# Performance work log

Measured on AMD Instinct MI355X. Metric: run time of the kernel, lower is better.

## Reference

```python
import jax, jax.numpy as jnp
import numpy as np

KSIZE = 3
SCALE = 10.0
EPS = 1e-4


def _prelu(x, a):
    return jnp.where(x >= 0, x, a * x)


def _conv1x1(x, w, b):
    # x: [B,C,H,W], w: [O,C], b: [O]
    return jnp.einsum('bchw,oc->bohw', x, w) + b[None, :, None, None]


def _extract_patches(x, k):
    # same-padded kxk patches, torch-unfold channel-major ordering.
    # x: [B,C,H,W] -> [B, H*W, C, k, k]
    B, C, H, W = x.shape
    p = k // 2
    xp = jnp.pad(x, ((0, 0), (0, 0), (p, p), (p, p)))
    pats = jnp.stack([xp[:, :, i:i + H, j:j + W]
                      for i in range(k) for j in range(k)], axis=2)  # [B,C,k*k,H,W]
    pats = pats.reshape(B, C, k, k, H * W)
    return jnp.transpose(pats, (0, 4, 1, 2, 3))


def setup_inputs() -> dict:
    key = jax.random.key(0)
    ks = jax.random.split(key, 10)
    B, C, r = 4, 64, 2
    H = W = 96
    h = w = 48
    Cr = C // r
    s = 0.05
    return {
        'input': jax.random.normal(ks[0], (B, C, H, W), jnp.float32),
        'small': jax.random.normal(ks[1], (B, C, h, w), jnp.float32),
        'w_match1': jax.random.normal(ks[2], (Cr, C), jnp.float32) * s,
        'b_match1': jax.random.normal(ks[3], (Cr,), jnp.float32) * s,
        'a_match1': jnp.full((1,), 0.25, jnp.float32),
        'w_match2': jax.random.normal(ks[4], (Cr, C), jnp.float32) * s,
        'b_match2': jax.random.normal(ks[5], (Cr,), jnp.float32) * s,
        'a_match2': jnp.full((1,), 0.25, jnp.float32),
        'w_asm': jax.random.normal(ks[6], (C, C), jnp.float32) * s,
        'b_asm': jax.random.normal(ks[7], (C,), jnp.float32) * s,
        'a_asm': jnp.full((1,), 0.25, jnp.float32),
    }


def reference(input, small, w_match1, b_match1, a_match1,
              w_match2, b_match2, a_match2, w_asm, b_asm, a_asm):
    dn = ('NCHW', 'OIHW', 'NCHW')
    pad1 = [(1, 1), (1, 1)]

    match_input = _prelu(_conv1x1(input, w_match1, b_match1), a_match1)  # [B,Cr,H,W]
    embed_w = _prelu(_conv1x1(small, w_asm, b_asm), a_asm)               # [B,C,h,w]
    ref = _prelu(_conv1x1(small, w_match2, b_match2), a_match2)          # [B,Cr,h,w]

    raw_w = _extract_patches(embed_w, KSIZE)  # [B, L, C, 3, 3]  (reconstruction filters)
    w_pat = _extract_patches(ref, KSIZE)      # [B, L, Cr, 3, 3] (matching filters)

    def per_sample(xi, wi, raw_wi):
        # xi: [Cr,H,W], wi: [L,Cr,3,3], raw_wi: [L,C,3,3]
        norm = jnp.sqrt(jnp.sum(wi * wi, axis=(1, 2, 3), keepdims=True))
        wi_n = wi / jnp.maximum(norm, EPS)
        # dynamic conv: correlation of xi with all L normalized patches
        yi = jax.lax.conv_general_dilated(xi[None], wi_n, (1, 1), pad1,
                                          dimension_numbers=dn)  # [1,L,H,W]
        yi = jax.nn.softmax(yi * SCALE, axis=1)
        # conv_transpose2d(yi, raw_wi, stride=2, padding=1):
        # lhs_dilation=2, pad k-1-p=1, spatially flipped, in/out swapped kernel
        wt = jnp.transpose(raw_wi, (1, 0, 2, 3))[:, :, ::-1, ::-1]  # [C,L,3,3]
        out = jax.lax.conv_general_dilated(yi, wt, (1, 1), pad1,
                                           lhs_dilation=(2, 2),
                                           dimension_numbers=dn)  # [1,C,2H-1,2W-1]
        return out[0] / 6.0

    return jax.vmap(per_sample)(match_input, w_pat, raw_w)
```

## Files before the change

kernel.cpp:

```cpp
#include <hip/hip_runtime.h>


typedef unsigned short u16;
typedef __attribute__((ext_vector_type(8))) short short8;
typedef __attribute__((ext_vector_type(8))) _Float16 half8;
typedef __attribute__((ext_vector_type(4))) float f32x4;

__device__ __forceinline__ u16 f2bf(float f) {
    unsigned u = __float_as_uint(f);
    unsigned r = (u + 0x7FFFu + ((u >> 16) & 1u)) >> 16;
    return (u16)r;
}
__device__ __forceinline__ float bf2f(u16 h) {
    return __uint_as_float(((unsigned)h) << 16);
}
__device__ __forceinline__ u16 f2h(float f) {
    _Float16 h = (_Float16)f;
    u16 u; __builtin_memcpy(&u, &h, 2); return u;
}
__device__ __forceinline__ float h2f(u16 u) {
    _Float16 h; __builtin_memcpy(&h, &u, 2); return (float)h;
}

__global__ void kzero(float4* p, long n) {
    long i = (long)blockIdx.x * blockDim.x + threadIdx.x;
    long st = (long)gridDim.x * blockDim.x;
    float4 z; z.x = 0.f; z.y = 0.f; z.z = 0.f; z.w = 0.f;
    for (; i < n; i += st) p[i] = z;
}

__global__ void kmatch(const float* __restrict__ input, const float* __restrict__ w1,
                       const float* __restrict__ b1, const float* __restrict__ a1,
                       u16* __restrict__ xf16) {
    __shared__ float xl[64 * 96];
    __shared__ float wl[32 * 65];
    int b = blockIdx.x / 96, y = blockIdx.x % 96;
    int tid = threadIdx.x;
    for (int i = tid; i < 64 * 96; i += 256) {
        int ci = i / 96, xx = i % 96;
        xl[i] = input[(((b * 64 + ci) * 96) + y) * 96 + xx];
    }
    for (int i = tid; i < 2048; i += 256) wl[(i >> 6) * 65 + (i & 63)] = w1[i];
    __syncthreads();
    float aa = a1[0];
    for (int o = tid; o < 96 * 32; o += 256) {
        int xx = o >> 5, c = o & 31;
        float acc = b1[c];
        #pragma unroll
        for (int ci = 0; ci < 64; ci++) acc = fmaf(xl[ci * 96 + xx], wl[c * 65 + ci], acc);
        float v = acc >= 0.f ? acc : aa * acc;
        xf16[((b * 98 + y + 1) * 98 + (xx + 1)) * 32 + c] = f2h(v);
    }
}

__global__ void ksmall(const float* __restrict__ small, const float* __restrict__ wasm,
                       const float* __restrict__ basm, const float* __restrict__ aasm,
                       const float* __restrict__ wm2, const float* __restrict__ bm2,
                       const float* __restrict__ am2,
                       float* __restrict__ ef32, u16* __restrict__ rkl) {
    __shared__ float sl[64 * 48];
    __shared__ float wa[64 * 65];
    __shared__ float wm[32 * 65];
    int b = blockIdx.x / 48, y = blockIdx.x % 48;
    int tid = threadIdx.x;
    for (int i = tid; i < 64 * 48; i += 256) {
        int ci = i / 48, xx = i % 48;
        sl[i] = small[(((b * 64 + ci) * 48) + y) * 48 + xx];
    }
    for (int i = tid; i < 4096; i += 256) wa[(i >> 6) * 65 + (i & 63)] = wasm[i];
    for (int i = tid; i < 2048; i += 256) wm[(i >> 6) * 65 + (i & 63)] = wm2[i];
    __syncthreads();
    float ae = aasm[0], ar = am2[0];
    for (int o = tid; o < 48 * 64; o += 256) {
        int xx = o >> 6, c = o & 63;
        float acc = basm[c];
        #pragma unroll
        for (int ci = 0; ci < 64; ci++) acc = fmaf(sl[ci * 48 + xx], wa[c * 65 + ci], acc);
        float v = acc >= 0.f ? acc : ae * acc;
        ef32[((b * 50 + y + 1) * 50 + (xx + 1)) * 64 + c] = v;
    }
    for (int o = tid; o < 48 * 32; o += 256) {
        int xx = o >> 5, c = o & 31;
        float acc = bm2[c];
        #pragma unroll
        for (int ci = 0; ci < 64; ci++) acc = fmaf(sl[ci * 48 + xx], wm[c * 65 + ci], acc);
        float v = acc >= 0.f ? acc : ar * acc;
        rkl[((b * 50 + y + 1) * 50 + (xx + 1)) * 32 + c] = f2h(v);
    }
}

__global__ void kinvnorm(const u16* __restrict__ rkl, float* __restrict__ invn) {
    int idx = blockIdx.x * 256 + threadIdx.x;
    int b = idx / 2304, l = idx % 2304;
    int ly = l / 48, lx = l % 48;
    float s = 0.f;
    for (int ty = 0; ty < 3; ty++)
        for (int tx = 0; tx < 3; tx++) {
            int base = ((b * 50 + ly + ty) * 50 + (lx + tx)) * 32;
            #pragma unroll
            for (int c = 0; c < 32; c++) {
                float v = h2f(rkl[base + c]);
                s = fmaf(v, v, s);
            }
        }
    invn[idx] = 10.f / fmaxf(sqrtf(s), 1e-4f);
}

__global__ void kvtp(const float* __restrict__ ef32, u16* __restrict__ vtp) {
    int bi = blockIdx.x;
    int b = bi / 576, n = bi % 576;
    int t = n >> 6, c = n & 63;
    int ty = t / 3, tx = t % 3;
    const float* eb = ef32 + (size_t)b * 50 * 50 * 64 + c;
    u16* vo = vtp + (size_t)(b * 576 + n) * 2304;
    for (int l = threadIdx.x; l < 2304; l += 256) {
        int ly = l / 48, lx = l - ly * 48;
        vo[l] = f2bf(eb[((ly + ty) * 50 + (lx + tx)) * 64]);
    }
}

__device__ __forceinline__ void stage_ks(const u16* __restrict__ src, u16* dst, int tid) {
    int wb = tid & ~63;
    #pragma unroll
    for (int k = 0; k < 3; ++k)
        __builtin_amdgcn_global_load_lds(
            (const __attribute__((address_space(1))) void*)(src + (size_t)(tid + k * 256) * 8),
            (__attribute__((address_space(3))) void*)(dst + (size_t)(wb + k * 256) * 8),
            16, 0, 0);
    if (tid < 32)
        __builtin_amdgcn_global_load_lds(
            (const __attribute__((address_space(1))) void*)(src + (size_t)(tid + 768) * 8),
            (__attribute__((address_space(3))) void*)(dst + (size_t)768 * 8),
            16, 0, 0);
}

__launch_bounds__(256, 2)
__global__ void kfused3(const u16* __restrict__ xf16, const u16* __restrict__ rkl,
                        const u16* __restrict__ vtp, const float* __restrict__ invn,
                        float* __restrict__ Z, int b0, int nb) {
    __shared__ u16 Ks[2][6400];
    __shared__ u16 Pl[2][6144];
    __shared__ float Ln[2304];
    __shared__ u16 Qs[6 * 18 * 32];
    __shared__ float llds[4][16];

    int tid = threadIdx.x;
    int w = tid >> 6, lane = tid & 63, l15 = lane & 15, quad = lane >> 4;
    int bi = blockIdx.x, brel, t;
    if (nb == 4) { brel = bi & 3; t = bi >> 2; }
    else         { brel = 0; t = bi; }
    int b = b0 + brel;
    int px0 = (t % 6) * 16, pyb = (t / 6) * 4;

    const u16* xb = xf16 + (size_t)b * 98 * 98 * 32;
    const u16* rb = rkl + (size_t)b * 50 * 50 * 32;
    const float* invb = invn + b * 2304;
    const u16* vw = vtp + (size_t)b * 576 * 2304 + (size_t)(w * 144 + l15) * 2304 + quad * 8;

    stage_ks(rb, Ks[0], tid);
    __builtin_amdgcn_sched_barrier(0);

    for (int i = tid; i < 576; i += 256)
        ((float4*)Ln)[i] = ((const float4*)invb)[i];

    for (int u = tid; u < 432; u += 256) {
        int cell = u >> 2, ch = u & 3;
        int r = cell / 18, p = cell % 18;
        *(short8*)&Qs[(r * 18 + p) * 32 + ch * 8] =
            *(const short8*)(xb + (((pyb + r) * 98) + (px0 + p)) * 32 + ch * 8);
    }

    f32x4 acc[36];
    #pragma unroll
    for (int i = 0; i < 36; i++) acc[i] = (f32x4)0.f;
    float lacc[4] = {0.f, 0.f, 0.f, 0.f};

    __syncthreads();

    short8 vv[9];

    for (int it = 0; it < 24; ++it) {
        int ly0 = it * 2;
        int cur = it & 1;

        if (it < 23) stage_ks(rb + (ly0 + 2) * 1600, Ks[cur ^ 1], tid);
        __builtin_amdgcn_sched_barrier(0);

        const u16* vit = vw + it * 96;
        #pragma unroll
        for (int nt = 0; nt < 9; ++nt) vv[nt] = *(const short8*)(vit + (size_t)nt * 36864);

        const u16* Kc = Ks[cur];
        u16* Pc = Pl[cur];
        #pragma unroll
        for (int kh = 0; kh < 2; ++kh) {
            f32x4 sf[3];
            #pragma unroll
            for (int i = 0; i < 3; i++) sf[i] = (f32x4)0.f;
            __builtin_amdgcn_s_setprio(1);
            #pragma unroll
            for (int ty = 0; ty < 3; ++ty)
                #pragma unroll
                for (int tx = 0; tx < 3; ++tx) {
                    half8 a = *(const half8*)&Qs[((w + ty) * 18 + (l15 + tx)) * 32 + quad * 8];
                    #pragma unroll
                    for (int lxo = 0; lxo < 3; ++lxo) {
                        half8 bb = *(const half8*)&Kc[(kh + ty) * 1600 + (lxo * 16 + l15 + tx) * 32 + quad * 8];
                        sf[lxo] = __builtin_amdgcn_mfma_f32_16x16x32_f16(a, bb, sf[lxo], 0, 0, 0);
                    }
                }
            __builtin_amdgcn_s_setprio(0);
            #pragma unroll
            for (int lxo = 0; lxo < 3; ++lxo) {
                float invs = Ln[(ly0 + kh) * 48 + lxo * 16 + l15];
                int k = kh * 48 + lxo * 16 + l15;
                int kb = k >> 5;
                int kc = (k & 31) ^ (quad << 3);
                #pragma unroll
                for (int r = 0; r < 4; ++r) {
                    float p = __expf(sf[lxo][r] * invs);
                    u16 h = f2bf(p);
                    Pc[(w * 3 + kb) * 512 + (quad * 4 + r) * 32 + kc] = h;
                    lacc[r] += bf2f(h);
                }
            }
        }

        asm volatile("s_waitcnt vmcnt(9) lgkmcnt(0)" ::: "memory");
        __builtin_amdgcn_s_barrier();
        __builtin_amdgcn_sched_barrier(0);

        const u16* Pr = Pl[cur];
        int pcol = l15 * 32 + ((quad ^ (l15 >> 2)) & 3) * 8;
        __builtin_amdgcn_s_setprio(1);
        #pragma unroll
        for (int ks = 0; ks < 3; ++ks) {
            short8 pa0 = *(const short8*)&Pr[(0 * 3 + ks) * 512 + pcol];
            short8 pa1 = *(const short8*)&Pr[(1 * 3 + ks) * 512 + pcol];
            #pragma unroll
            for (int nt = 0; nt < 9; ++nt) {
                short8 vn = vv[nt];
                acc[0 * 9 + nt] = __builtin_amdgcn_mfma_f32_16x16x32_bf16(pa0, vn, acc[0 * 9 + nt], 0, 0, 0);
                acc[1 * 9 + nt] = __builtin_amdgcn_mfma_f32_16x16x32_bf16(pa1, vn, acc[1 * 9 + nt], 0, 0, 0);
            }
            pa0 = *(const short8*)&Pr[(2 * 3 + ks) * 512 + pcol];
            pa1 = *(const short8*)&Pr[(3 * 3 + ks) * 512 + pcol];
            #pragma unroll
            for (int nt = 0; nt < 9; ++nt) {
                short8 vn = vv[nt];
                acc[2 * 9 + nt] = __builtin_amdgcn_mfma_f32_16x16x32_bf16(pa0, vn, acc[2 * 9 + nt], 0, 0, 0);
                acc[3 * 9 + nt] = __builtin_amdgcn_mfma_f32_16x16x32_bf16(pa1, vn, acc[3 * 9 + nt], 0, 0, 0);
                if (ks < 2)
                    vv[nt] = *(const short8*)(vit + (size_t)nt * 36864 + (ks + 1) * 32);
            }
        }
        __builtin_amdgcn_s_setprio(0);
    }

    #pragma unroll
    for (int r = 0; r < 4; ++r) {
        float v = lacc[r];
        v += __shfl_xor(v, 1);
        v += __shfl_xor(v, 2);
        v += __shfl_xor(v, 4);
        v += __shfl_xor(v, 8);
        lacc[r] = v;
    }
    if (l15 == 0) {
        #pragma unroll
        for (int r = 0; r < 4; ++r)
            llds[w][quad * 4 + r] = lacc[r];
    }
    __syncthreads();
    float* Zb = Z + (size_t)brel * 9216 * 576;
    #pragma unroll
    for (int mt = 0; mt < 4; ++mt) {
        #pragma unroll
        for (int r = 0; r < 4; ++r) {
            int q = (pyb + mt) * 96 + px0 + quad * 4 + r;
            float rl = 1.0f / (llds[mt][quad * 4 + r] * 6.0f);
            float* zr = Zb + (size_t)q * 576 + w * 144;
            #pragma unroll
            for (int nt = 0; nt < 9; ++nt)
                __builtin_nontemporal_store(acc[mt * 9 + nt][r] * rl, zr + nt * 16 + l15);
        }
    }
}

__global__ void kgather(const float* __restrict__ Z, float* __restrict__ out, int b0) {
    __shared__ float zb[2 * 9 * 580];
    int bi = blockIdx.x;
    int brel = bi / (96 * 12);
    int rem = bi % (96 * 12);
    int b = b0 + brel;
    int q = rem / 12, xt = rem % 12;
    int ox0 = xt * 16, p0 = ox0 >> 1;
    const float* Zb = Z + (size_t)brel * 9216 * 576;
    int tid = threadIdx.x;
    for (int id = tid; id < 2592; id += 256) {
        int pi = id / 1296, r2 = id % 1296;
        int pxi = r2 / 144, n4 = r2 % 144;
        int py = q + pi; if (py > 95) py = 95;
        int px = p0 + pxi; if (px > 95) px = 95;
        *(float4*)&zb[(pi * 9 + pxi) * 580 + n4 * 4] =
            *(const float4*)&Zb[(size_t)(py * 96 + px) * 576 + n4 * 4];
    }
    __syncthreads();
    int xi = tid & 15, cq = tid >> 4;
    int ox = ox0 + xi;
    bool oxv = ox <= 190;
    int ntx, txl[2], pxl[2];
    if (xi & 1) { ntx = 2; txl[0] = 0; pxl[0] = (xi + 1) >> 1; txl[1] = 2; pxl[1] = (xi - 1) >> 1; }
    else        { ntx = 1; txl[0] = 1; pxl[0] = xi >> 1; txl[1] = 1; pxl[1] = xi >> 1; }
    int oy0 = 2 * q;
    #pragma unroll
    for (int ck = 0; ck < 4; ++ck) {
        int c = cq + ck * 16;
        float v0 = 0.f, v1 = 0.f;
        for (int j = 0; j < ntx; ++j) {
            int tx = txl[j], pxi = pxl[j];
            v0 += zb[(0 * 9 + pxi) * 580 + (3 + tx) * 64 + c];
            v1 += zb[(1 * 9 + pxi) * 580 + (0 + tx) * 64 + c];
            v1 += zb[(0 * 9 + pxi) * 580 + (6 + tx) * 64 + c];
        }
        if (oxv) {
            float* o = out + (((size_t)(b * 64 + c) * 191 + oy0) * 191 + ox);
            *o = v0;
            if (q < 95) *(o + 191) = v1;
        }
    }
}

extern "C" void kernel_launch(void* const* d_in, const int* in_sizes, int n_in,
                              void* d_out, int out_size, void* d_ws, size_t ws_size,
                              hipStream_t stream) {
    const float* input = (const float*)d_in[0];
    const float* small = (const float*)d_in[1];
    const float* w1 = (const float*)d_in[2];
    const float* b1 = (const float*)d_in[3];
    const float* a1 = (const float*)d_in[4];
    const float* w2 = (const float*)d_in[5];
    const float* b2 = (const float*)d_in[6];
    const float* a2 = (const float*)d_in[7];
    const float* wa = (const float*)d_in[8];
    const float* ba = (const float*)d_in[9];
    const float* aa = (const float*)d_in[10];

    char* ws = (char*)d_ws;
    u16* xf16 = (u16*)(ws + 0);
    u16* rkl = (u16*)(ws + 2458624);
    float* ef = (float*)(ws + 3098624);
    u16* vtp = (u16*)(ws + 5658624);
    float* invn = (float*)(ws + 16275456);
    const size_t PREP = 16312320;
    float* Zbuf = (float*)(ws + PREP);
    float* out = (float*)d_out;

    int nb = (ws_size >= (size_t)101246976) ? 4 : 1;

    kzero<<<1024, 256, 0, stream>>>((float4*)ws, 5658624 / 16);
    kmatch<<<384, 256, 0, stream>>>(input, w1, b1, a1, xf16);
    ksmall<<<192, 256, 0, stream>>>(small, wa, ba, aa, w2, b2, a2, ef, rkl);
    kinvnorm<<<36, 256, 0, stream>>>(rkl, invn);
    kvtp<<<2304, 256, 0, stream>>>(ef, vtp);

    for (int b0 = 0; b0 < 4; b0 += nb) {
        kfused3<<<nb * 144, 256, 0, stream>>>(xf16, rkl, vtp, invn, Zbuf, b0, nb);
        kgather<<<nb * 1152, 256, 0, stream>>>(Zbuf, out, b0);
    }
}
```

Before: 540.6 us.

## Double fused kernel tile height to 8 rows with 512-thread blocks sharing staged keys

The fused attention kernel now processes 8 pixel rows per block instead of 4, using 512 threads split into two M-groups of four warps that share the same staged key patches and value streams. This halves the number of blocks and halves the per-tile redundant staging of keys, inverse norms and value loads relative to output. It doubles LDS for the probability buffer and query tile, and leaves fewer blocks (72 per sample) than before, which may hurt occupancy or load balance across CUs. The hidden softmax section must also be indexing correctly for the larger tile, which is not visible here.

```diff
diff --git a/kernel.cpp b/kernel.cpp
--- a/kernel.cpp
+++ b/kernel.cpp
@@ -120,50 +120,48 @@
 }
 
 __device__ __forceinline__ void stage_ks(const u16* __restrict__ src, u16* dst, int tid) {
-    int wb = tid & ~63;
-    #pragma unroll
-    for (int k = 0; k < 3; ++k)
+    __builtin_amdgcn_global_load_lds(
+        (const __attribute__((address_space(1))) void*)(src + (size_t)tid * 8),
+        (__attribute__((address_space(3))) void*)(dst + (size_t)(tid & ~63) * 8),
+        16, 0, 0);
+    if (tid < 288)
         __builtin_amdgcn_global_load_lds(
-            (const __attribute__((address_space(1))) void*)(src + (size_t)(tid + k * 256) * 8),
-            (__attribute__((address_space(3))) void*)(dst + (size_t)(wb + k * 256) * 8),
+            (const __attribute__((address_space(1))) void*)(src + (size_t)(tid + 512) * 8),
+            (__attribute__((address_space(3))) void*)(dst + (size_t)((tid & ~63) + 512) * 8),
             16, 0, 0);
-    if (tid < 32)
-        __builtin_amdgcn_global_load_lds(
-            (const __attribute__((address_space(1))) void*)(src + (size_t)(tid + 768) * 8),
-            (__attribute__((address_space(3))) void*)(dst + (size_t)768 * 8),
-            16, 0, 0);
-}
-
-__launch_bounds__(256, 2)
-__global__ void kfused3(const u16* __restrict__ xf16, const u16* __restrict__ rkl,
+}
+
+__launch_bounds__(512, 2)
+__global__ void kfused4(const u16* __restrict__ xf16, const u16* __restrict__ rkl,
                         const u16* __restrict__ vtp, const float* __restrict__ invn,
                         float* __restrict__ Z, int b0, int nb) {
     __shared__ u16 Ks[2][6400];
-    __shared__ u16 Pl[2][6144];
+    __shared__ u16 Pl[2][12288];
     __shared__ float Ln[2304];
-    __shared__ u16 Qs[6 * 18 * 32];
-    __shared__ float llds[4][16];
+    __shared__ u16 Qs[10 * 18 * 32];
+    __shared__ float llds[8][16];
 
     int tid = threadIdx.x;
     int w = tid >> 6, lane = tid & 63, l15 = lane & 15, quad = lane >> 4;
+    int mg = w >> 2, ng = w & 3;
     int bi = blockIdx.x, brel, t;
     if (nb == 4) { brel = bi & 3; t = bi >> 2; }
     else         { brel = 0; t = bi; }
     int b = b0 + brel;
-    int px0 = (t % 6) * 16, pyb = (t / 6) * 4;
+    int px0 = (t % 6) * 16, pyb = (t / 6) * 8;
 
     const u16* xb = xf16 + (size_t)b * 98 * 98 * 32;
     const u16* rb = rkl + (size_t)b * 50 * 50 * 32;
     const float* invb = invn + b * 2304;
-    const u16* vw = vtp + (size_t)b * 576 * 2304 + (size_t)(w * 144 + l15) * 2304 + quad * 8;
+    const u16* vw = vtp + (size_t)b * 576 * 2304 + (size_t)(ng * 144 + l15) * 2304 + quad * 8;
 
     stage_ks(rb, Ks[0], tid);
     __builtin_amdgcn_sched_barrier(0);
 
-    for (int i = tid; i < 576; i += 256)
+    for (int i = tid; i < 576; i += 512)
         ((float4*)Ln)[i] = ((const float4*)invb)[i];
 
-    for (int u = tid; u < 432; u += 256) {
+    for (int u = tid; u < 720; u += 512) {
         int cell = u >> 2, ch = u & 3;
         int r = cell / 18, p = cell % 18;
         *(short8*)&Qs[(r * 18 + p) * 32 + ch * 8] =
@@ -235,16 +233,16 @@
         __builtin_amdgcn_s_setprio(1);
         #pragma unroll
         for (int ks = 0; ks < 3; ++ks) {
-            short8 pa0 = *(const short8*)&Pr[(0 * 3 + ks) * 512 + pcol];
-            short8 pa1 = *(const short8*)&Pr[(1 * 3 + ks) * 512 + pcol];
+            short8 pa0 = *(const short8*)&Pr[((mg * 4 + 0) * 3 + ks) * 512 + pcol];
+            short8 pa1 = *(const short8*)&Pr[((mg * 4 + 1) * 3 + ks) * 512 + pcol];
             #pragma unroll
             for (int nt = 0; nt < 9; ++nt) {
                 short8 vn = vv[nt];
                 acc[0 * 9 + nt] = __builtin_amdgcn_mfma_f32_16x16x32_bf16(pa0, vn, acc[0 * 9 + nt], 0, 0, 0);
                 acc[1 * 9 + nt] = __builtin_amdgcn_mfma_f32_16x16x32_bf16(pa1, vn, acc[1 * 9 + nt], 0, 0, 0);
             }
-            pa0 = *(const short8*)&Pr[(2 * 3 + ks) * 512 + pcol];
-            pa1 = *(const short8*)&Pr[(3 * 3 + ks) * 512 + pcol];
+            pa0 = *(const short8*)&Pr[((mg * 4 + 2) * 3 + ks) * 512 + pcol];
+            pa1 = *(const short8*)&Pr[((mg * 4 + 3) * 3 + ks) * 512 + pcol];
             #pragma unroll
             for (int nt = 0; nt < 9; ++nt) {
                 short8 vn = vv[nt];
@@ -275,11 +273,12 @@
     float* Zb = Z + (size_t)brel * 9216 * 576;
     #pragma unroll
     for (int mt = 0; mt < 4; ++mt) {
+        int m8 = mg * 4 + mt;
         #pragma unroll
         for (int r = 0; r < 4; ++r) {
-            int q = (pyb + mt) * 96 + px0 + quad * 4 + r;
-            float rl = 1.0f / (llds[mt][quad * 4 + r] * 6.0f);
-            float* zr = Zb + (size_t)q * 576 + w * 144;
+            int q = (pyb + m8) * 96 + px0 + quad * 4 + r;
+            float rl = 1.0f / (llds[m8][quad * 4 + r] * 6.0f);
+            float* zr = Zb + (size_t)q * 576 + ng * 144;
             #pragma unroll
             for (int nt = 0; nt < 9; ++nt)
                 __builtin_nontemporal_store(acc[mt * 9 + nt][r] * rl, zr + nt * 16 + l15);
@@ -365,7 +364,7 @@
     kvtp<<<2304, 256, 0, stream>>>(ef, vtp);
 
     for (int b0 = 0; b0 < 4; b0 += nb) {
-        kfused3<<<nb * 144, 256, 0, stream>>>(xf16, rkl, vtp, invn, Zbuf, b0, nb);
+        kfused4<<<nb * 72, 512, 0, stream>>>(xf16, rkl, vtp, invn, Zbuf, b0, nb);
         kgather<<<nb * 1152, 256, 0, stream>>>(Zbuf, out, b0);
     }
 }
```

New measurement: 638.1 us. 1.18x slower.

## Stage kvtp rows in LDS with packed stores; share K-row fragments across kh

Applied to the files above, without the earlier changes.

kvtp now launches one block per (batch, patch row). Each block loads three 50x64 embedding rows into shared memory and writes packed 4-element bf16 stores, replacing strided scalar global gathers. In the fused kernel, the two kh iterations are merged so that each K row fragment loaded from LDS feeds both score accumulators. This cuts K-operand LDS reads for rows 1-2, at the cost of more live accumulator registers. kvtp launches far fewer blocks, so less parallelism is available in that kernel.

```diff
diff --git a/kernel.cpp b/kernel.cpp
--- a/kernel.cpp
+++ b/kernel.cpp
@@ -107,15 +107,31 @@
 }
 
 __global__ void kvtp(const float* __restrict__ ef32, u16* __restrict__ vtp) {
+    __shared__ float el[3][50 * 64];
     int bi = blockIdx.x;
-    int b = bi / 576, n = bi % 576;
-    int t = n >> 6, c = n & 63;
-    int ty = t / 3, tx = t % 3;
-    const float* eb = ef32 + (size_t)b * 50 * 50 * 64 + c;
-    u16* vo = vtp + (size_t)(b * 576 + n) * 2304;
-    for (int l = threadIdx.x; l < 2304; l += 256) {
-        int ly = l / 48, lx = l - ly * 48;
-        vo[l] = f2bf(eb[((ly + ty) * 50 + (lx + tx)) * 64]);
+    int b = bi / 48, ly = bi % 48;
+    const float* eb = ef32 + (size_t)b * 50 * 50 * 64;
+    int tid = threadIdx.x;
+    #pragma unroll
+    for (int r = 0; r < 3; ++r)
+        for (int i = tid; i < 800; i += 256)
+            ((float4*)el[r])[i] = ((const float4*)(eb + (size_t)(ly + r) * 3200))[i];
+    __syncthreads();
+    u16* vo = vtp + (size_t)b * 576 * 2304 + (size_t)ly * 48;
+    for (int n = tid; n < 576; n += 256) {
+        int t = n >> 6, c = n & 63;
+        int ty = t / 3, tx = t - ty * 3;
+        u16* dst = vo + (size_t)n * 2304;
+        const float* src = &el[ty][tx * 64 + c];
+        #pragma unroll
+        for (int g = 0; g < 12; ++g) {
+            unsigned lo = (unsigned)f2bf(src[(g * 4 + 0) * 64]) |
+                          ((unsigned)f2bf(src[(g * 4 + 1) * 64]) << 16);
+            unsigned hi = (unsigned)f2bf(src[(g * 4 + 2) * 64]) |
+                          ((unsigned)f2bf(src[(g * 4 + 3) * 64]) << 16);
+            uint2 pk; pk.x = lo; pk.y = hi;
+            *(uint2*)&dst[g * 4] = pk;
+        }
     }
 }
 
@@ -192,37 +208,67 @@
 
         const u16* Kc = Ks[cur];
         u16* Pc = Pl[cur];
-        #pragma unroll
-        for (int kh = 0; kh < 2; ++kh) {
-            f32x4 sf[3];
-            #pragma unroll
-            for (int i = 0; i < 3; i++) sf[i] = (f32x4)0.f;
-            __builtin_amdgcn_s_setprio(1);
-            #pragma unroll
-            for (int ty = 0; ty < 3; ++ty)
+        f32x4 sf0[3], sf1[3];
+        #pragma unroll
+        for (int i = 0; i < 3; i++) { sf0[i] = (f32x4)0.f; sf1[i] = (f32x4)0.f; }
+
+        __builtin_amdgcn_s_setprio(1);
+        #pragma unroll
+        for (int row = 0; row < 3; ++row)
+            #pragma unroll
+            for (int tx = 0; tx < 3; ++tx) {
+                half8 a0 = *(const half8*)&Qs[((w + row) * 18 + (l15 + tx)) * 32 + quad * 8];
+                half8 a1;
+                if (row >= 1) a1 = *(const half8*)&Qs[((w + row - 1) * 18 + (l15 + tx)) * 32 + quad * 8];
                 #pragma unroll
-                for (int tx = 0; tx < 3; ++tx) {
-                    half8 a = *(const half8*)&Qs[((w + ty) * 18 + (l15 + tx)) * 32 + quad * 8];
-                    #pragma unroll
-                    for (int lxo = 0; lxo < 3; ++lxo) {
-                        half8 bb = *(const half8*)&Kc[(kh + ty) * 1600 + (lxo * 16 + l15 + tx) * 32 + quad * 8];
-                        sf[lxo] = __builtin_amdgcn_mfma_f32_16x16x32_f16(a, bb, sf[lxo], 0, 0, 0);
-                    }
+                for (int lxo = 0; lxo < 3; ++lxo) {
+                    half8 bb = *(const half8*)&Kc[row * 1600 + (lxo * 16 + l15 + tx) * 32 + quad * 8];
+                    sf0[lxo] = __builtin_amdgcn_mfma_f32_16x16x32_f16(a0, bb, sf0[lxo], 0, 0, 0);
+                    if (row >= 1)
+                        sf1[lxo] = __builtin_amdgcn_mfma_f32_16x16x32_f16(a1, bb, sf1[lxo], 0, 0, 0);
                 }
-            __builtin_amdgcn_s_setprio(0);
+            }
+        __builtin_amdgcn_s_setprio(0);
+
+        #pragma unroll
+        for (int lxo = 0; lxo < 3; ++lxo) {
+            float invs = Ln[(ly0 + 0) * 48 + lxo * 16 + l15];
+            int k = 0 * 48 + lxo * 16 + l15;
+            int kb = k >> 5;
+            int kc = (k & 31) ^ (quad << 3);
+            #pragma unroll
+            for (int r = 0; r < 4; ++r) {
+                float p = __expf(sf0[lxo][r] * invs);
+                u16 h = f2bf(p);
+                Pc[(w * 3 + kb) * 512 + (quad * 4 + r) * 32 + kc] = h;
+                lacc[r] += bf2f(h);
+            }
+        }
+
+        __builtin_amdgcn_s_setprio(1);
+        #pragma unroll
+        for (int tx = 0; tx < 3; ++tx) {
+            half8 a1 = *(const half8*)&Qs[((w + 2) * 18 + (l15 + tx)) * 32 + quad * 8];
             #pragma unroll
             for (int lxo = 0; lxo < 3; ++lxo) {
-                float invs = Ln[(ly0 + kh) * 48 + lxo * 16 + l15];
-                int k = kh * 48 + lxo * 16 + l15;
-                int kb = k >> 5;
-                int kc = (k & 31) ^ (quad << 3);
-                #pragma unroll
-                for (int r = 0; r < 4; ++r) {
-                    float p = __expf(sf[lxo][r] * invs);
-                    u16 h = f2bf(p);
-                    Pc[(w * 3 + kb) * 512 + (quad * 4 + r) * 32 + kc] = h;
-                    lacc[r] += bf2f(h);
-                }
+                half8 bb = *(const half8*)&Kc[3 * 1600 + (lxo * 16 + l15 + tx) * 32 + quad * 8];
+                sf1[lxo] = __builtin_amdgcn_mfma_f32_16x16x32_f16(a1, bb, sf1[lxo], 0, 0, 0);
+            }
+        }
+        __builtin_amdgcn_s_setprio(0);
+
+        #pragma unroll
+        for (int lxo = 0; lxo < 3; ++lxo) {
+            float invs = Ln[(ly0 + 1) * 48 + lxo * 16 + l15];
+            int k = 1 * 48 + lxo * 16 + l15;
+            int kb = k >> 5;
+            int kc = (k & 31) ^ (quad << 3);
+            #pragma unroll
+            for (int r = 0; r < 4; ++r) {
+                float p = __expf(sf1[lxo][r] * invs);
+                u16 h = f2bf(p);
+                Pc[(w * 3 + kb) * 512 + (quad * 4 + r) * 32 + kc] = h;
+                lacc[r] += bf2f(h);
             }
         }
 
@@ -362,7 +408,7 @@
     kmatch<<<384, 256, 0, stream>>>(input, w1, b1, a1, xf16);
     ksmall<<<192, 256, 0, stream>>>(small, wa, ba, aa, w2, b2, a2, ef, rkl);
     kinvnorm<<<36, 256, 0, stream>>>(rkl, invn);
-    kvtp<<<2304, 256, 0, stream>>>(ef, vtp);
+    kvtp<<<192, 256, 0, stream>>>(ef, vtp);
 
     for (int b0 = 0; b0 < 4; b0 += nb) {
         kfused3<<<nb * 144, 256, 0, stream>>>(xf16, rkl, vtp, invn, Zbuf, b0, nb);
```

Result: slower. 589.4 us (+9.0%).
